# Performance work log

Measured on AMD Instinct MI355X. Metric: run time of the kernel, lower is better.

The kernel has to match this reference:

```python
import jax, jax.numpy as jnp
import numpy as np

B, DM, H, W = 4, 192, 48, 48
DI = 2 * DM          # d_inner = d_expand (ssm_ratio=ssm_rank_ratio=2)
K, N, R = 4, 16, 12  # directions, d_state, dt_rank=ceil(192/16)
L = H * W
EPS = 1e-5


def setup_inputs() -> dict:
    key = jax.random.key(0)
    ks = jax.random.split(key, 10)
    f = lambda k, s, sc: (sc * jax.random.normal(k, s)).astype(jnp.float32)
    return {
        "x": jax.random.normal(ks[0], (B, DM, H, W), jnp.float32),
        "in_proj_w": f(ks[1], (2 * DI, DM), 0.05),        # Conv2d 1x1, bias=False
        "conv_w": f(ks[2], (DI, 1, 3, 3), 0.1),           # depthwise 3x3
        "conv_b": f(ks[3], (DI,), 0.1),
        "x_proj_weight": f(ks[4], (K, R + 2 * N, DI), 0.05),
        "dt_projs_weight": f(ks[5], (K, DI, R), 0.1),
        "dt_projs_bias": f(ks[6], (K, DI), 0.5),
        "A_logs": f(ks[7], (K * DI, N), 0.5),
        "Ds": jnp.ones((K * DI,), jnp.float32),
        "ln_w": jnp.ones((DI,), jnp.float32),
        "ln_b": jnp.zeros((DI,), jnp.float32),
        "out_proj_w": f(ks[8], (DM, DI), 0.05),           # Conv2d 1x1, bias=False
    }


def selective_scan(u, delta, A, Bs, Cs, Ds):
    # u, delta: (B,K,D,L); A: (K,D,N); Bs, Cs: (B,K,N,L); Ds: (K,D)
    uT = jnp.moveaxis(u, -1, 0)
    dT = jnp.moveaxis(delta, -1, 0)
    BT = jnp.moveaxis(Bs, -1, 0)
    CT = jnp.moveaxis(Cs, -1, 0)
    h0 = jnp.zeros(u.shape[:3] + (A.shape[-1],), u.dtype)  # (B,K,D,N)

    def step(h, inp):
        u_l, d_l, B_l, C_l = inp  # (B,K,D),(B,K,D),(B,K,N),(B,K,N)
        dA = jnp.exp(d_l[..., None] * A)                    # (B,K,D,N)
        h = h * dA + (d_l * u_l)[..., None] * B_l[:, :, None, :]
        y = jnp.einsum("bkdn,bkn->bkd", h, C_l)
        return h, y

    _, ys = jax.lax.scan(step, h0, (uT, dT, BT, CT))       # ys: (L,B,K,D)
    ys = jnp.moveaxis(ys, 0, -1)                            # (B,K,D,L)
    return ys + u * Ds[None, :, :, None]


def _forward(x, in_proj_w, conv_w, conv_b, x_proj_weight, dt_projs_weight,
             dt_projs_bias, A_logs, Ds, ln_w, ln_b, out_proj_w):
    # in_proj (1x1 conv) -> split x / z; z branch gets exact GELU
    xz = jnp.einsum("od,bdhw->bohw", in_proj_w, x)
    xc, z = jnp.split(xz, 2, axis=1)
    z1 = jax.nn.gelu(z, approximate=False)
    # depthwise 3x3 conv + GELU
    xc = jax.lax.conv_general_dilated(
        xc, conv_w, (1, 1), "SAME",
        feature_group_count=DI,
        dimension_numbers=("NCHW", "OIHW", "NCHW"),
    ) + conv_b[None, :, None, None]
    xc = jax.nn.gelu(xc, approximate=False)
    # CrossScan: row-major, col-major, and their reversals -> (B,K,D,L)
    x0 = xc.reshape(B, DI, L)
    x1 = jnp.swapaxes(xc, 2, 3).reshape(B, DI, L)
    xs = jnp.stack([x0, x1, x0[..., ::-1], x1[..., ::-1]], axis=1)
    # per-direction projections
    x_dbl = jnp.einsum("bkdl,kcd->bkcl", xs, x_proj_weight)
    dts, Bs, Cs = jnp.split(x_dbl, [R, R + N], axis=2)      # (B,K,R,L),(B,K,N,L)x2
    dts = jnp.einsum("bkrl,kdr->bkdl", dts, dt_projs_weight)
    delta = jax.nn.softplus(dts + dt_projs_bias[None, :, :, None])
    A = -jnp.exp(A_logs.reshape(K, DI, N))
    ys = selective_scan(xs, delta, A, Bs, Cs, Ds.reshape(K, DI))
    # CrossMerge: un-flip, fold col-major branch back to row-major
    y02 = ys[:, 0] + ys[:, 2, :, ::-1]
    y13 = ys[:, 1] + ys[:, 3, :, ::-1]
    y = y02 + jnp.swapaxes(y13.reshape(B, DI, W, H), 2, 3).reshape(B, DI, L)
    # out_norm (LayerNorm over channel) in (B,H,W,D)
    y = y.reshape(B, DI, H, W).transpose(0, 2, 3, 1)
    mu = y.mean(-1, keepdims=True)
    var = ((y - mu) ** 2).mean(-1, keepdims=True)
    y = (y - mu) / jnp.sqrt(var + EPS) * ln_w + ln_b
    # gate with z, out_proj 1x1
    y = y.transpose(0, 3, 1, 2) * z1
    return jnp.einsum("od,bdhw->bohw", out_proj_w, y)


def reference(x, in_proj_w, conv_w, conv_b, x_proj_weight, dt_projs_weight,
              dt_projs_bias, A_logs, Ds, ln_w, ln_b, out_proj_w):
    return _forward(x, in_proj_w, conv_w, conv_b, x_proj_weight,
                    dt_projs_weight, dt_projs_bias, A_logs, Ds,
                    ln_w, ln_b, out_proj_w)
```

## Files before the change

kernel.cpp:

```cpp
#include <hip/hip_runtime.h>
#include <math.h>

#define BQ 4
#define DM 192
#define DI 384
#define HH 48
#define WW 48
#define LL 2304
#define KK 4
#define NN 16
#define RR 12
#define CH 48
#define CLEN 48

#define LOG2E 1.4426950408889634f

typedef short v8s __attribute__((ext_vector_type(8)));
typedef float v4f __attribute__((ext_vector_type(4)));

__device__ __forceinline__ float gelu_exact(float x) {
    return 0.5f * x * (1.0f + erff(x * 0.7071067811865476f));
}

__device__ __forceinline__ float softplus_f(float x) {
    return fmaxf(x, 0.0f) + log1pf(expf(-fabsf(x)));
}

__device__ __forceinline__ int pos_for(int k, int l) {
    if (k == 0) return l;
    if (k == 1) { return (l % HH) * WW + (l / HH); }
    if (k == 2) return (LL - 1) - l;
    int j = (LL - 1) - l;
    return (j % HH) * WW + (j / HH);
}

__device__ __forceinline__ int pt_of(int p) {
    return (p % 48) * 48 + p / 48;
}

__device__ __forceinline__ float fexp2(float x) {
    return __builtin_amdgcn_exp2f(x);
}

__device__ __forceinline__ short f2bf(float x) {
    unsigned u = __float_as_uint(x);
    unsigned r = (u + 0x7FFFu + ((u >> 16) & 1u)) >> 16;
    return (short)r;
}

template<int CTRL>
__device__ __forceinline__ float dpp_movf(float v) {
    return __int_as_float(__builtin_amdgcn_update_dpp(
        0, __float_as_int(v), CTRL, 0xF, 0xF, true));
}

__global__ __launch_bounds__(256) void k_prep_w(const float* __restrict__ ipw,
                                                const float* __restrict__ opw,
                                                const float* __restrict__ xpw,
                                                short* __restrict__ wibf,
                                                short* __restrict__ owbf,
                                                short* __restrict__ wpbf) {
    int i = blockIdx.x * 256 + threadIdx.x;
    if (i < 147456)       wibf[i] = f2bf(ipw[i]);
    else if (i < 221184)  owbf[i - 147456] = f2bf(opw[i - 147456]);
    else if (i < 288768)  wpbf[i - 221184] = f2bf(xpw[i - 221184]);
    else                  wpbf[67584 + (i - 288768)] = 0;
}

__global__ __launch_bounds__(256) void k_prep_xT(const float* __restrict__ x,
                                                 short* __restrict__ xTbf) {
    __shared__ float T[32][33];
    int blk = blockIdx.x;
    int dt = blk % 6;
    int lt = (blk / 6) % 72;
    int b  = blk / (6 * 72);
    int d0 = dt * 32, l0 = lt * 32;
    int tx = threadIdx.x & 31, ty = threadIdx.x >> 5;
    #pragma unroll
    for (int i = 0; i < 4; ++i) {
        int dd = ty + 8 * i;
        T[dd][tx] = x[(size_t)(b * DM + d0 + dd) * LL + l0 + tx];
    }
    __syncthreads();
    #pragma unroll
    for (int i = 0; i < 4; ++i) {
        int ll = ty + 8 * i;
        xTbf[(size_t)(b * LL + l0 + ll) * DM + d0 + tx] = f2bf(T[tx][ll]);
    }
}

__global__ __launch_bounds__(256) void k_inproj_mfma(
    const short* __restrict__ xTbf,
    const short* __restrict__ wibf,
    float* __restrict__ xcz)
{
    __shared__ short sA[128 * 40];
    __shared__ short sB[64 * 40];
    int o0 = blockIdx.x * 64;
    int l0 = blockIdx.y * 128;
    int b  = blockIdx.z;
    int tid = threadIdx.x;
    int lane = tid & 63, wid = tid >> 6;
    int n = lane & 15, quad = lane >> 4;

    v4f acc[2][4];
    #pragma unroll
    for (int i = 0; i < 2; ++i)
        #pragma unroll
        for (int j = 0; j < 4; ++j) acc[i][j] = (v4f){0.f, 0.f, 0.f, 0.f};

    for (int kc = 0; kc < 192; kc += 32) {
        for (int i = tid; i < 512; i += 256) {
            int row = i >> 2, seg = i & 3;
            *(v8s*)&sA[row * 40 + seg * 8] =
                *(const v8s*)(xTbf + (size_t)(b * LL + l0 + row) * DM + kc + seg * 8);
        }
        {
            int row = tid >> 2, seg = tid & 3;
            *(v8s*)&sB[row * 40 + seg * 8] =
                *(const v8s*)(wibf + (size_t)(o0 + row) * DM + kc + seg * 8);
        }
        __syncthreads();
        v8s a0 = *(v8s*)&sA[(wid * 32 + n) * 40 + quad * 8];
        v8s a1 = *(v8s*)&sA[(wid * 32 + 16 + n) * 40 + quad * 8];
        #pragma unroll
        for (int os = 0; os < 4; ++os) {
            v8s bv = *(v8s*)&sB[(os * 16 + n) * 40 + quad * 8];
            acc[0][os] = __builtin_amdgcn_mfma_f32_16x16x32_bf16(a0, bv, acc[0][os], 0, 0, 0);
            acc[1][os] = __builtin_amdgcn_mfma_f32_16x16x32_bf16(a1, bv, acc[1][os], 0, 0, 0);
        }
        __syncthreads();
    }
    bool zhalf = (o0 >= DI);
    #pragma unroll
    for (int ls = 0; ls < 2; ++ls)
        #pragma unroll
        for (int os = 0; os < 4; ++os) {
            int o = o0 + os * 16 + n;
            #pragma unroll
            for (int r = 0; r < 4; ++r) {
                int l = l0 + wid * 32 + ls * 16 + quad * 4 + r;
                float v = acc[ls][os][r];
                xcz[(size_t)(b * LL + l) * 768 + o] = zhalf ? gelu_exact(v) : v;
            }
        }
}

__global__ __launch_bounds__(384) void k_dwconv(const float* __restrict__ xcz,
                                                const float* __restrict__ cw,
                                                const float* __restrict__ cb,
                                                float* __restrict__ xcT,
                                                short* __restrict__ xcTbf) {
    int blk = blockIdx.x;
    int seg = blk & 3;
    int bh = blk >> 2;
    int b = bh / HH, h = bh % HH;
    int d = threadIdx.x;
    int w0 = seg * 12;
    const float* in = xcz + (size_t)b * LL * 768 + d;
    float w9[9];
    #pragma unroll
    for (int i = 0; i < 9; ++i) w9[i] = cw[d * 9 + i];
    float bias = cb[d];
    bool hm = h > 0, hp = h < HH - 1;
    int r0 = (h - 1) * WW, r1 = h * WW, r2 = (h + 1) * WW;
    float c00, c01, c02, c10, c11, c12, c20, c21, c22;
    bool wl = (w0 > 0);
    c00 = (hm && wl) ? in[(size_t)(r0 + w0 - 1) * 768] : 0.f;
    c10 = wl ? in[(size_t)(r1 + w0 - 1) * 768] : 0.f;
    c20 = (hp && wl) ? in[(size_t)(r2 + w0 - 1) * 768] : 0.f;
    c01 = hm ? in[(size_t)(r0 + w0) * 768] : 0.f;
    c11 = in[(size_t)(r1 + w0) * 768];
    c21 = hp ? in[(size_t)(r2 + w0) * 768] : 0.f;
    c02 = hm ? in[(size_t)(r0 + w0 + 1) * 768] : 0.f;
    c12 = in[(size_t)(r1 + w0 + 1) * 768];
    c22 = hp ? in[(size_t)(r2 + w0 + 1) * 768] : 0.f;
    #pragma unroll
    for (int wi = 0; wi < 12; ++wi) {
        int w = w0 + wi;
        float s = bias
            + w9[0] * c00 + w9[1] * c01 + w9[2] * c02
            + w9[3] * c10 + w9[4] * c11 + w9[5] * c12
            + w9[6] * c20 + w9[7] * c21 + w9[8] * c22;
        float v = gelu_exact(s);
        size_t row = (size_t)(b * LL + h * WW + w);
        xcT[row * DI + d] = v;
        xcTbf[row * DI + d] = f2bf(v);
        c00 = c01; c01 = c02; c10 = c11; c11 = c12; c20 = c21; c21 = c22;
        int wn = w + 2;
        bool okw = wn < WW;
        c02 = (hm && okw) ? in[(size_t)(r0 + wn) * 768] : 0.f;
        c12 = okw ? in[(size_t)(r1 + wn) * 768] : 0.f;
        c22 = (hp && okw) ? in[(size_t)(r2 + wn) * 768] : 0.f;
    }
}

__global__ __launch_bounds__(256) void k_xproj_mfma(
    const short* __restrict__ xcTbf,
    const short* __restrict__ wpbf,
    float* __restrict__ dts,
    float* __restrict__ Bsb,
    float* __restrict__ Csb)
{
    __shared__ short sA[128 * 40];
    __shared__ short sB[64 * 40];
    int o0 = blockIdx.x * 64;
    int l0 = blockIdx.y * 128;
    int b  = blockIdx.z;
    int tid = threadIdx.x;
    int lane = tid & 63, wid = tid >> 6;
    int n = lane & 15, quad = lane >> 4;

    v4f acc[2][4];
    #pragma unroll
    for (int i = 0; i < 2; ++i)
        #pragma unroll
        for (int j = 0; j < 4; ++j) acc[i][j] = (v4f){0.f, 0.f, 0.f, 0.f};

    for (int kc = 0; kc < DI; kc += 32) {
        for (int i = tid; i < 512; i += 256) {
            int row = i >> 2, seg = i & 3;
            *(v8s*)&sA[row * 40 + seg * 8] =
                *(const v8s*)(xcTbf + (size_t)(b * LL + l0 + row) * DI + kc + seg * 8);
        }
        {
            int row = tid >> 2, seg = tid & 3;
            *(v8s*)&sB[row * 40 + seg * 8] =
                *(const v8s*)(wpbf + (size_t)(o0 + row) * DI + kc + seg * 8);
        }
        __syncthreads();
        v8s a0 = *(v8s*)&sA[(wid * 32 + n) * 40 + quad * 8];
        v8s a1 = *(v8s*)&sA[(wid * 32 + 16 + n) * 40 + quad * 8];
        #pragma unroll
        for (int os = 0; os < 4; ++os) {
            v8s bv = *(v8s*)&sB[(os * 16 + n) * 40 + quad * 8];
            acc[0][os] = __builtin_amdgcn_mfma_f32_16x16x32_bf16(a0, bv, acc[0][os], 0, 0, 0);
            acc[1][os] = __builtin_amdgcn_mfma_f32_16x16x32_bf16(a1, bv, acc[1][os], 0, 0, 0);
        }
        __syncthreads();
    }
    #pragma unroll
    for (int ls = 0; ls < 2; ++ls)
        #pragma unroll
        for (int os = 0; os < 4; ++os) {
            int c_all = o0 + os * 16 + n;
            if (c_all >= 176) continue;
            int k = c_all / 44;
            int c = c_all - k * 44;
            int bk = b * 4 + k;
            #pragma unroll
            for (int r = 0; r < 4; ++r) {
                int lp = l0 + wid * 32 + ls * 16 + quad * 4 + r;
                int lk = (k == 0) ? lp
                       : (k == 1) ? pt_of(lp)
                       : (k == 2) ? (LL - 1 - lp)
                                  : (LL - 1 - pt_of(lp));
                float v = acc[ls][os][r];
                size_t base = (size_t)bk * LL + lk;
                if (c < RR)           dts[base * RR + c] = v;
                else if (c < RR + NN) Bsb[base * NN + (c - RR)] = v;
                else                  Csb[base * NN + (c - RR - NN)] = v;
            }
        }
}

__global__ __launch_bounds__(256, 6) void k_scan_pass1(
    const float* __restrict__ xcT,
    const float* __restrict__ dts,
    const float* __restrict__ Bsb,
    const float* __restrict__ Csb,
    const float* __restrict__ dtw_g,
    const float* __restrict__ dtb_g,
    const float* __restrict__ Alogs,
    const float* __restrict__ Ds_g,
    float* __restrict__ Sbuf,
    float* __restrict__ hstin,
    float* __restrict__ yk)
{
    __shared__ float sB[CLEN * 16];
    __shared__ float sC[CLEN * 16];
    __shared__ float sDts[CLEN * 12];
    __shared__ float sDel[CLEN * 64];

    int blk = blockIdx.x;
    int dblk = blk % 6;
    int tmp = blk / 6;
    int c = tmp % CH;
    int bk = tmp / CH;
    int k = bk & 3, b = bk >> 2;
    int tid = threadIdx.x;
    int l0 = c * CLEN;

    {
        const float4* Bg = (const float4*)(Bsb + ((size_t)bk * LL + l0) * NN);
        const float4* Cg = (const float4*)(Csb + ((size_t)bk * LL + l0) * NN);
        if (tid < CLEN * 4) {
            ((float4*)sB)[tid] = Bg[tid];
            ((float4*)sC)[tid] = Cg[tid];
        }
        const float4* Dg = (const float4*)(dts + ((size_t)bk * LL + l0) * RR);
        for (int i = tid; i < CLEN * 3; i += 256)
            ((float4*)sDts)[i] = Dg[i];
    }
    __syncthreads();
    {
        int dl = tid & 63, lset = tid >> 6;
        int dd = dblk * 64 + dl;
        int kdq = k * DI + dd;
        float dtbv = dtb_g[kdq];
        float w12[12];
        {
            const float4* p = (const float4*)(dtw_g + (size_t)kdq * RR);
            float4 a0 = p[0], a1 = p[1], a2 = p[2];
            w12[0]=a0.x; w12[1]=a0.y; w12[2]=a0.z;  w12[3]=a0.w;
            w12[4]=a1.x; w12[5]=a1.y; w12[6]=a1.z;  w12[7]=a1.w;
            w12[8]=a2.x; w12[9]=a2.y; w12[10]=a2.z; w12[11]=a2.w;
        }
        #pragma unroll
        for (int j = 0; j < 12; ++j) {
            int l = lset * 12 + j;
            const float* dp = sDts + l * 12;
            float acc = dtbv;
            #pragma unroll
            for (int r = 0; r < 12; ++r) acc += dp[r] * w12[r];
            sDel[l * 64 + dl] = softplus_f(acc);
        }
    }
    __syncthreads();

    int lane = tid & 63, wv = tid >> 6;
    int q = lane & 3;
    int d16 = lane >> 2;
    int dl = wv * 16 + d16;
    int d = dblk * 64 + dl;
    int kd = k * DI + d;
    int n0 = q << 2;

    float4 Al = *(const float4*)(Alogs + (size_t)kd * NN + n0);
    float A2[4] = { -expf(Al.x) * LOG2E, -expf(Al.y) * LOG2E,
                    -expf(Al.z) * LOG2E, -expf(Al.w) * LOG2E };
    float Dv = Ds_g[kd];
    float* Sc = Sbuf + ((size_t)bk * LL + l0 + q) * DI + d;
    float* yc = yk   + ((size_t)bk * LL + l0 + q) * DI + d;

    int pbase = (k == 0) ? l0
              : (k == 1) ? c
              : (k == 2) ? (LL - 1 - l0)
                         : (LL - 1 - c);
    int pstep = (k == 0) ? 1 : (k == 1) ? WW : (k == 2) ? -1 : -WW;
    const float* up = xcT + ((size_t)b * LL + pbase) * DI + d;
    int ustep = pstep * DI;

    float h0 = 0.f, h1 = 0.f, h2 = 0.f, h3 = 0.f;
    float td = 0.f;
    float yhold = 0.f, Shold = 0.f;

    #pragma unroll
    for (int l = 0; l < CLEN; ++l) {
        float delta = sDel[l * 64 + dl];
        float ub_b  = *up;
        up += ustep;
        td += delta;
        float du = delta * ub_b;
        float4 B4 = *(const float4*)&sB[l * 16 + n0];
        h0 = h0 * fexp2(delta * A2[0]) + du * B4.x;
        h1 = h1 * fexp2(delta * A2[1]) + du * B4.y;
        h2 = h2 * fexp2(delta * A2[2]) + du * B4.z;
        h3 = h3 * fexp2(delta * A2[3]) + du * B4.w;
        float4 C4 = *(const float4*)&sC[l * 16 + n0];
        float yp = h0 * C4.x + h1 * C4.y + h2 * C4.z + h3 * C4.w;
        yp += dpp_movf<0xB1>(yp);
        yp += dpp_movf<0x4E>(yp);
        float yf = yp + ub_b * Dv;
        if (q == (l & 3)) { yhold = yf; Shold = td; }
        if ((l & 3) == 3) {
            *yc = yhold; *Sc = Shold;
            yc += 4 * DI; Sc += 4 * DI;
        }
    }

    float4 h4; h4.x = h0; h4.y = h1; h4.z = h2; h4.w = h3;
    *(float4*)(hstin + ((size_t)(bk * CH + c) * DI + d) * NN + n0) = h4;
}

__global__ __launch_bounds__(256) void k_scan_combine(
    float* __restrict__ hstin,
    const float* __restrict__ Sbuf,
    const float* __restrict__ Alogs)
{
    int t = blockIdx.x * 256 + threadIdx.x;
    int n = t & 15;
    int d = (t >> 4) % DI;
    int bk = t / (DI * NN);
    int k = bk & 3;
    float A2 = -expf(Alogs[(size_t)(k * DI + d) * NN + n]) * LOG2E;
    float h = 0.f;
    for (int c = 0; c < CH; ++c) {
        size_t rb = (size_t)(bk * CH + c) * DI + d;
        float hend = hstin[rb * NN + n];
        hstin[rb * NN + n] = h;
        float St = Sbuf[((size_t)bk * LL + c * CLEN + CLEN - 1) * DI + d];
        h = fexp2(A2 * St) * h + hend;
    }
}

__global__ __launch_bounds__(256, 6) void k_corr(
    const float* __restrict__ Csb,
    const float* __restrict__ Sbuf,
    const float* __restrict__ hin,
    const float* __restrict__ Alogs,
    float* __restrict__ yk)
{
    __shared__ float sC[CLEN * 16];

    int blk = blockIdx.x;
    int dblk = blk % 6;
    int tmp = blk / 6;
    int c = tmp % CH;
    if (c == 0) return;
    int bk = tmp / CH;
    int k = bk & 3;
    int tid = threadIdx.x;
    int l0 = c * CLEN;

    {
        const float4* Cg = (const float4*)(Csb + ((size_t)bk * LL + l0) * NN);
        if (tid < CLEN * 4) ((float4*)sC)[tid] = Cg[tid];
    }
    __syncthreads();

    int lane = tid & 63, wv = tid >> 6;
    int q = lane & 3;
    int d16 = lane >> 2;
    int dl = wv * 16 + d16;
    int d = dblk * 64 + dl;
    int kd = k * DI + d;
    int n0 = q << 2;

    float4 Al = *(const float4*)(Alogs + (size_t)kd * NN + n0);
    float A2[4] = { -expf(Al.x) * LOG2E, -expf(Al.y) * LOG2E,
                    -expf(Al.z) * LOG2E, -expf(Al.w) * LOG2E };
    float4 H4 = *(const float4*)(hin + ((size_t)(bk * CH + c) * DI + d) * NN + n0);
    float* yc = yk + ((size_t)bk * LL + l0 + q) * DI + d;
    const float* Sp = Sbuf + ((size_t)bk * LL + l0) * DI + d;

    float ychold = 0.f;
    #pragma unroll
    for (int l = 0; l < CLEN; ++l) {
        float S = *Sp;
        Sp += DI;
        float4 C4 = *(const float4*)&sC[l * 16 + n0];
        float yv = C4.x * fexp2(A2[0] * S) * H4.x
                 + C4.y * fexp2(A2[1] * S) * H4.y
                 + C4.z * fexp2(A2[2] * S) * H4.z
                 + C4.w * fexp2(A2[3] * S) * H4.w;
        yv += dpp_movf<0xB1>(yv);
        yv += dpp_movf<0x4E>(yv);
        if (q == (l & 3)) ychold = yv;
        if ((l & 3) == 3) {
            *yc += ychold;
            yc += 4 * DI;
        }
    }
}

__global__ __launch_bounds__(384) void k_merge_ln_gate(
    const float* __restrict__ yk,
    const float* __restrict__ xcz,
    const float* __restrict__ lnw,
    const float* __restrict__ lnb,
    short* __restrict__ gbufb)
{
    int pg = blockIdx.x;
    int b = pg / LL;
    int pos = pg % LL;
    int d = threadIdx.x;
    int pt = (pos % 48) * 48 + pos / 48;

    const float* y0 = yk + ((size_t)(b * 4 + 0) * LL + pos) * DI;
    const float* y1 = yk + ((size_t)(b * 4 + 1) * LL + pt) * DI;
    const float* y2 = yk + ((size_t)(b * 4 + 2) * LL + (LL - 1 - pos)) * DI;
    const float* y3 = yk + ((size_t)(b * 4 + 3) * LL + (LL - 1 - pt)) * DI;
    float v = y0[d] + y1[d] + y2[d] + y3[d];

    float s = v, qq = v * v;
    #pragma unroll
    for (int o = 32; o >= 1; o >>= 1) {
        s += __shfl_xor(s, o, 64);
        qq += __shfl_xor(qq, o, 64);
    }
    __shared__ float ssum[6], sqq[6];
    int lane = d & 63, w = d >> 6;
    if (lane == 0) { ssum[w] = s; sqq[w] = qq; }
    __syncthreads();
    float ts = 0.f, tq = 0.f;
    #pragma unroll
    for (int i = 0; i < 6; ++i) { ts += ssum[i]; tq += sqq[i]; }
    float mu = ts / (float)DI;
    float var = tq / (float)DI - mu * mu;
    float inv = rsqrtf(var + 1e-5f);
    float y = (v - mu) * inv * lnw[d] + lnb[d];
    float z = xcz[(size_t)pg * 768 + DI + d];
    gbufb[(size_t)pg * DI + d] = f2bf(y * z);
}

__global__ __launch_bounds__(256) void k_outproj_mfma(
    const short* __restrict__ gbufb,
    const short* __restrict__ owbf,
    float* __restrict__ out)
{
    __shared__ short sA[128 * 40];
    __shared__ short sB[64 * 40];
    int o0 = blockIdx.x * 64;
    int l0 = blockIdx.y * 128;
    int b  = blockIdx.z;
    int tid = threadIdx.x;
    int lane = tid & 63, wid = tid >> 6;
    int n = lane & 15, quad = lane >> 4;

    v4f acc[2][4];
    #pragma unroll
    for (int i = 0; i < 2; ++i)
        #pragma unroll
        for (int j = 0; j < 4; ++j) acc[i][j] = (v4f){0.f, 0.f, 0.f, 0.f};

    for (int kc = 0; kc < DI; kc += 32) {
        for (int i = tid; i < 512; i += 256) {
            int row = i >> 2, seg = i & 3;
            *(v8s*)&sA[row * 40 + seg * 8] =
                *(const v8s*)(gbufb + (size_t)(b * LL + l0 + row) * DI + kc + seg * 8);
        }
        {
            int row = tid >> 2, seg = tid & 3;
            *(v8s*)&sB[row * 40 + seg * 8] =
                *(const v8s*)(owbf + (size_t)(o0 + row) * DI + kc + seg * 8);
        }
        __syncthreads();
        v8s a0 = *(v8s*)&sA[(wid * 32 + n) * 40 + quad * 8];
        v8s a1 = *(v8s*)&sA[(wid * 32 + 16 + n) * 40 + quad * 8];
        #pragma unroll
        for (int os = 0; os < 4; ++os) {
            v8s bv = *(v8s*)&sB[(os * 16 + n) * 40 + quad * 8];
            acc[0][os] = __builtin_amdgcn_mfma_f32_16x16x32_bf16(a0, bv, acc[0][os], 0, 0, 0);
            acc[1][os] = __builtin_amdgcn_mfma_f32_16x16x32_bf16(a1, bv, acc[1][os], 0, 0, 0);
        }
        __syncthreads();
    }
    #pragma unroll
    for (int ls = 0; ls < 2; ++ls)
        #pragma unroll
        for (int os = 0; os < 4; ++os) {
            int o = o0 + os * 16 + n;
            #pragma unroll
            for (int r = 0; r < 4; ++r) {
                int l = l0 + wid * 32 + ls * 16 + quad * 4 + r;
                out[(size_t)(b * DM + o) * LL + l] = acc[ls][os][r];
            }
        }
}

extern "C" void kernel_launch(void* const* d_in, const int* in_sizes, int n_in,
                              void* d_out, int out_size, void* d_ws, size_t ws_size,
                              hipStream_t stream) {
    (void)in_sizes; (void)n_in; (void)out_size; (void)ws_size;
    const float* x      = (const float*)d_in[0];
    const float* ipw    = (const float*)d_in[1];
    const float* cw     = (const float*)d_in[2];
    const float* cb     = (const float*)d_in[3];
    const float* xpw    = (const float*)d_in[4];
    const float* dtw    = (const float*)d_in[5];
    const float* dtb    = (const float*)d_in[6];
    const float* Alogs  = (const float*)d_in[7];
    const float* Ds     = (const float*)d_in[8];
    const float* lnw    = (const float*)d_in[9];
    const float* lnb    = (const float*)d_in[10];
    const float* opw    = (const float*)d_in[11];
    float* out = (float*)d_out;

    float* wsf = (float*)d_ws;
    const size_t XCZ = (size_t)BQ * LL * 768;
    const size_t SZ  = (size_t)BQ * DI * LL;
    const size_t DTS = (size_t)BQ * KK * LL * RR;
    const size_t BCS = (size_t)BQ * KK * LL * NN;
    const size_t SBF = (size_t)BQ * KK * LL * DI;
    const size_t HST = (size_t)BQ * KK * CH * DI * NN;

    float* xcz   = wsf;
    float* xcT   = xcz + XCZ;
    float* dts   = xcT + SZ;
    float* Bsb   = dts + DTS;
    float* Csb   = Bsb + BCS;
    float* Sbuf  = Csb + BCS;
    float* hstin = Sbuf + SBF;
    float* yk    = hstin + HST;
    short* xTbf  = (short*)(yk + SBF);
    short* wibf  = xTbf + (size_t)BQ * LL * DM;
    short* owbf  = wibf + 768 * 192;
    short* wpbf  = owbf + 192 * 384;
    short* gbufb = (short*)Sbuf;
    short* xcTbf = (short*)yk;

    k_prep_w<<<1152, 256, 0, stream>>>(ipw, opw, xpw, wibf, owbf, wpbf);
    k_prep_xT<<<BQ * 72 * 6, 256, 0, stream>>>(x, xTbf);
    k_inproj_mfma<<<dim3(12, 18, BQ), 256, 0, stream>>>(xTbf, wibf, xcz);
    k_dwconv<<<BQ * HH * 4, 384, 0, stream>>>(xcz, cw, cb, xcT, xcTbf);
    k_xproj_mfma<<<dim3(3, 18, BQ), 256, 0, stream>>>(xcTbf, wpbf, dts, Bsb, Csb);

    k_scan_pass1<<<BQ * KK * CH * 6, 256, 0, stream>>>(
        xcT, dts, Bsb, Csb, dtw, dtb, Alogs, Ds, Sbuf, hstin, yk);
    k_scan_combine<<<(BQ * KK * DI * NN) / 256, 256, 0, stream>>>(
        hstin, Sbuf, Alogs);
    k_corr<<<BQ * KK * CH * 6, 256, 0, stream>>>(Csb, Sbuf, hstin, Alogs, yk);
    k_merge_ln_gate<<<BQ * LL, 384, 0, stream>>>(yk, xcz, lnw, lnb, gbufb);

    k_outproj_mfma<<<dim3(3, 18, BQ), 256, 0, stream>>>(gbufb, owbf, out);
}
```

Before: 297.0 us.

## Replace scan correction pass with full rescan seeded by chunk carry-in state

Pass 1 of the chunked selective scan now computes only the end-of-chunk state and the per-chunk delta sum, and no longer writes y or per-step cumulative delta (Sbuf). Pass 2 reruns the whole recurrence from the carry-in state and writes the final y directly, replacing the correction kernel that read Sbuf and did read-modify-write on yk. This removes a large per-step cumulative-delta buffer and its write and read traffic, in exchange for recomputing delta, softplus and the recurrence twice. Chunk 0 blocks now do work in pass 2 as well.

```diff
diff --git a/kernel.cpp b/kernel.cpp
--- a/kernel.cpp
+++ b/kernel.cpp
@@ -24,14 +24,6 @@
 
 __device__ __forceinline__ float softplus_f(float x) {
     return fmaxf(x, 0.0f) + log1pf(expf(-fabsf(x)));
-}
-
-__device__ __forceinline__ int pos_for(int k, int l) {
-    if (k == 0) return l;
-    if (k == 1) { return (l % HH) * WW + (l / HH); }
-    if (k == 2) return (LL - 1) - l;
-    int j = (LL - 1) - l;
-    return (j % HH) * WW + (j / HH);
 }
 
 __device__ __forceinline__ int pt_of(int p) {
@@ -268,17 +260,13 @@
     const float* __restrict__ xcT,
     const float* __restrict__ dts,
     const float* __restrict__ Bsb,
-    const float* __restrict__ Csb,
     const float* __restrict__ dtw_g,
     const float* __restrict__ dtb_g,
     const float* __restrict__ Alogs,
-    const float* __restrict__ Ds_g,
-    float* __restrict__ Sbuf,
     float* __restrict__ hstin,
-    float* __restrict__ yk)
+    float* __restrict__ Tsum)
 {
     __shared__ float sB[CLEN * 16];
-    __shared__ float sC[CLEN * 16];
     __shared__ float sDts[CLEN * 12];
     __shared__ float sDel[CLEN * 64];
 
@@ -293,11 +281,7 @@
 
     {
         const float4* Bg = (const float4*)(Bsb + ((size_t)bk * LL + l0) * NN);
-        const float4* Cg = (const float4*)(Csb + ((size_t)bk * LL + l0) * NN);
-        if (tid < CLEN * 4) {
-            ((float4*)sB)[tid] = Bg[tid];
-            ((float4*)sC)[tid] = Cg[tid];
-        }
+        if (tid < CLEN * 4) ((float4*)sB)[tid] = Bg[tid];
         const float4* Dg = (const float4*)(dts + ((size_t)bk * LL + l0) * RR);
         for (int i = tid; i < CLEN * 3; i += 256)
             ((float4*)sDts)[i] = Dg[i];
@@ -339,9 +323,6 @@
     float4 Al = *(const float4*)(Alogs + (size_t)kd * NN + n0);
     float A2[4] = { -expf(Al.x) * LOG2E, -expf(Al.y) * LOG2E,
                     -expf(Al.z) * LOG2E, -expf(Al.w) * LOG2E };
-    float Dv = Ds_g[kd];
-    float* Sc = Sbuf + ((size_t)bk * LL + l0 + q) * DI + d;
-    float* yc = yk   + ((size_t)bk * LL + l0 + q) * DI + d;
 
     int pbase = (k == 0) ? l0
               : (k == 1) ? c
@@ -353,7 +334,6 @@
 
     float h0 = 0.f, h1 = 0.f, h2 = 0.f, h3 = 0.f;
     float td = 0.f;
-    float yhold = 0.f, Shold = 0.f;
 
     #pragma unroll
     for (int l = 0; l < CLEN; ++l) {
@@ -367,25 +347,16 @@
         h1 = h1 * fexp2(delta * A2[1]) + du * B4.y;
         h2 = h2 * fexp2(delta * A2[2]) + du * B4.z;
         h3 = h3 * fexp2(delta * A2[3]) + du * B4.w;
-        float4 C4 = *(const float4*)&sC[l * 16 + n0];
-        float yp = h0 * C4.x + h1 * C4.y + h2 * C4.z + h3 * C4.w;
-        yp += dpp_movf<0xB1>(yp);
-        yp += dpp_movf<0x4E>(yp);
-        float yf = yp + ub_b * Dv;
-        if (q == (l & 3)) { yhold = yf; Shold = td; }
-        if ((l & 3) == 3) {
-            *yc = yhold; *Sc = Shold;
-            yc += 4 * DI; Sc += 4 * DI;
-        }
     }
 
     float4 h4; h4.x = h0; h4.y = h1; h4.z = h2; h4.w = h3;
     *(float4*)(hstin + ((size_t)(bk * CH + c) * DI + d) * NN + n0) = h4;
+    if (q == 0) Tsum[(size_t)(bk * CH + c) * DI + d] = td;
 }
 
 __global__ __launch_bounds__(256) void k_scan_combine(
     float* __restrict__ hstin,
-    const float* __restrict__ Sbuf,
+    const float* __restrict__ Tsum,
     const float* __restrict__ Alogs)
 {
     int t = blockIdx.x * 256 + threadIdx.x;
@@ -399,33 +370,71 @@
         size_t rb = (size_t)(bk * CH + c) * DI + d;
         float hend = hstin[rb * NN + n];
         hstin[rb * NN + n] = h;
-        float St = Sbuf[((size_t)bk * LL + c * CLEN + CLEN - 1) * DI + d];
+        float St = Tsum[rb];
         h = fexp2(A2 * St) * h + hend;
     }
 }
 
-__global__ __launch_bounds__(256, 6) void k_corr(
+__global__ __launch_bounds__(256, 6) void k_scan_pass2(
+    const float* __restrict__ xcT,
+    const float* __restrict__ dts,
+    const float* __restrict__ Bsb,
     const float* __restrict__ Csb,
-    const float* __restrict__ Sbuf,
+    const float* __restrict__ dtw_g,
+    const float* __restrict__ dtb_g,
+    const float* __restrict__ Alogs,
+    const float* __restrict__ Ds_g,
     const float* __restrict__ hin,
-    const float* __restrict__ Alogs,
     float* __restrict__ yk)
 {
+    __shared__ float sB[CLEN * 16];
     __shared__ float sC[CLEN * 16];
+    __shared__ float sDts[CLEN * 12];
+    __shared__ float sDel[CLEN * 64];
 
     int blk = blockIdx.x;
     int dblk = blk % 6;
     int tmp = blk / 6;
     int c = tmp % CH;
-    if (c == 0) return;
     int bk = tmp / CH;
-    int k = bk & 3;
+    int k = bk & 3, b = bk >> 2;
     int tid = threadIdx.x;
     int l0 = c * CLEN;
 
     {
+        const float4* Bg = (const float4*)(Bsb + ((size_t)bk * LL + l0) * NN);
         const float4* Cg = (const float4*)(Csb + ((size_t)bk * LL + l0) * NN);
-        if (tid < CLEN * 4) ((float4*)sC)[tid] = Cg[tid];
+        if (tid < CLEN * 4) {
+            ((float4*)sB)[tid] = Bg[tid];
+            ((float4*)sC)[tid] = Cg[tid];
+        }
+        const float4* Dg = (const float4*)(dts + ((size_t)bk * LL + l0) * RR);
+        for (int i = tid; i < CLEN * 3; i += 256)
+            ((float4*)sDts)[i] = Dg[i];
+    }
+    __syncthreads();
+    {
+        int dl = tid & 63, lset = tid >> 6;
+        int dd = dblk * 64 + dl;
+        int kdq = k * DI + dd;
+        float dtbv = dtb_g[kdq];
+        float w12[12];
+        {
+            const float4* p = (const float4*)(dtw_g + (size_t)kdq * RR);
+            float4 a0 = p[0], a1 = p[1], a2 = p[2];
+            w12[0]=a0.x; w12[1]=a0.y; w12[2]=a0.z;  w12[3]=a0.w;
+            w12[4]=a1.x; w12[5]=a1.y; w12[6]=a1.z;  w12[7]=a1.w;
+            w12[8]=a2.x; w12[9]=a2.y; w12[10]=a2.z; w12[11]=a2.w;
+        }
+        #pragma unroll
+        for (int j = 0; j < 12; ++j) {
+            int l = lset * 12 + j;
+            const float* dp = sDts + l * 12;
+            float acc = dtbv;
+            #pragma unroll
+            for (int r = 0; r < 12; ++r) acc += dp[r] * w12[r];
+            sDel[l * 64 + dl] = softplus_f(acc);
+        }
     }
     __syncthreads();
 
@@ -440,25 +449,40 @@
     float4 Al = *(const float4*)(Alogs + (size_t)kd * NN + n0);
     float A2[4] = { -expf(Al.x) * LOG2E, -expf(Al.y) * LOG2E,
                     -expf(Al.z) * LOG2E, -expf(Al.w) * LOG2E };
+    float Dv = Ds_g[kd];
+    float* yc = yk + ((size_t)bk * LL + l0 + q) * DI + d;
+
+    int pbase = (k == 0) ? l0
+              : (k == 1) ? c
+              : (k == 2) ? (LL - 1 - l0)
+                         : (LL - 1 - c);
+    int pstep = (k == 0) ? 1 : (k == 1) ? WW : (k == 2) ? -1 : -WW;
+    const float* up = xcT + ((size_t)b * LL + pbase) * DI + d;
+    int ustep = pstep * DI;
+
     float4 H4 = *(const float4*)(hin + ((size_t)(bk * CH + c) * DI + d) * NN + n0);
-    float* yc = yk + ((size_t)bk * LL + l0 + q) * DI + d;
-    const float* Sp = Sbuf + ((size_t)bk * LL + l0) * DI + d;
-
-    float ychold = 0.f;
+    float h0 = H4.x, h1 = H4.y, h2 = H4.z, h3 = H4.w;
+    float yhold = 0.f;
+
     #pragma unroll
     for (int l = 0; l < CLEN; ++l) {
-        float S = *Sp;
-        Sp += DI;
+        float delta = sDel[l * 64 + dl];
+        float ub_b  = *up;
+        up += ustep;
+        float du = delta * ub_b;
+        float4 B4 = *(const float4*)&sB[l * 16 + n0];
+        h0 = h0 * fexp2(delta * A2[0]) + du * B4.x;
+        h1 = h1 * fexp2(delta * A2[1]) + du * B4.y;
+        h2 = h2 * fexp2(delta * A2[2]) + du * B4.z;
+        h3 = h3 * fexp2(delta * A2[3]) + du * B4.w;
         float4 C4 = *(const float4*)&sC[l * 16 + n0];
-        float yv = C4.x * fexp2(A2[0] * S) * H4.x
-                 + C4.y * fexp2(A2[1] * S) * H4.y
-                 + C4.z * fexp2(A2[2] * S) * H4.z
-                 + C4.w * fexp2(A2[3] * S) * H4.w;
-        yv += dpp_movf<0xB1>(yv);
-        yv += dpp_movf<0x4E>(yv);
-        if (q == (l & 3)) ychold = yv;
+        float yp = h0 * C4.x + h1 * C4.y + h2 * C4.z + h3 * C4.w;
+        yp += dpp_movf<0xB1>(yp);
+        yp += dpp_movf<0x4E>(yp);
+        float yf = yp + ub_b * Dv;
+        if (q == (l & 3)) yhold = yf;
         if ((l & 3) == 3) {
-            *yc += ychold;
+            *yc = yhold;
             yc += 4 * DI;
         }
     }
@@ -582,6 +606,7 @@
     const size_t SZ  = (size_t)BQ * DI * LL;
     const size_t DTS = (size_t)BQ * KK * LL * RR;
     const size_t BCS = (size_t)BQ * KK * LL * NN;
+    const size_t TSM = (size_t)BQ * KK * CH * DI;
     const size_t SBF = (size_t)BQ * KK * LL * DI;
     const size_t HST = (size_t)BQ * KK * CH * DI * NN;
 
@@ -590,14 +615,14 @@
     float* dts   = xcT + SZ;
     float* Bsb   = dts + DTS;
     float* Csb   = Bsb + BCS;
-    float* Sbuf  = Csb + BCS;
-    float* hstin = Sbuf + SBF;
+    float* Tsum  = Csb + BCS;
+    float* hstin = Tsum + TSM;
     float* yk    = hstin + HST;
     short* xTbf  = (short*)(yk + SBF);
     short* wibf  = xTbf + (size_t)BQ * LL * DM;
     short* owbf  = wibf + 768 * 192;
     short* wpbf  = owbf + 192 * 384;
-    short* gbufb = (short*)Sbuf;
+    short* gbufb = wpbf + 192 * 384;
     short* xcTbf = (short*)yk;
 
     k_prep_w<<<1152, 256, 0, stream>>>(ipw, opw, xpw, wibf, owbf, wpbf);
@@ -607,10 +632,11 @@
     k_xproj_mfma<<<dim3(3, 18, BQ), 256, 0, stream>>>(xcTbf, wpbf, dts, Bsb, Csb);
 
     k_scan_pass1<<<BQ * KK * CH * 6, 256, 0, stream>>>(
-        xcT, dts, Bsb, Csb, dtw, dtb, Alogs, Ds, Sbuf, hstin, yk);
+        xcT, dts, Bsb, dtw, dtb, Alogs, hstin, Tsum);
     k_scan_combine<<<(BQ * KK * DI * NN) / 256, 256, 0, stream>>>(
-        hstin, Sbuf, Alogs);
-    k_corr<<<BQ * KK * CH * 6, 256, 0, stream>>>(Csb, Sbuf, hstin, Alogs, yk);
+        hstin, Tsum, Alogs);
+    k_scan_pass2<<<BQ * KK * CH * 6, 256, 0, stream>>>(
+        xcT, dts, Bsb, Csb, dtw, dtb, Alogs, Ds, hstin, yk);
     k_merge_ln_gate<<<BQ * LL, 384, 0, stream>>>(yk, xcz, lnw, lnb, gbufb);
 
     k_outproj_mfma<<<dim3(3, 18, BQ), 256, 0, stream>>>(gbufb, owbf, out);
```

Result: slower. 337.1 us (+13.5%).
